# Optimization experiments

Measured on AMD Instinct MI355X. Metric: run time of the kernel, lower is better.

The kernel has to match this reference:

```python
import jax, jax.numpy as jnp
import numpy as np

B, S, D, F, E, R, K = 1, 512, 1024, 4096, 8, 16, 2
SCALING = 32.0 / 16.0  # lora_alpha / lora_r
EPS = 1e-6


def setup_inputs() -> dict:
    key = jax.random.key(0)
    ks = jax.random.split(key, 12)
    w = lambda k, shape: jax.random.normal(k, shape, dtype=jnp.float32) * 0.02
    return {
        "x": jax.random.normal(ks[0], (B, S, D), dtype=jnp.float32),
        "norm_w": jnp.ones((D,), jnp.float32),
        "w1": w(ks[1], (F, D)),      # up proj (gate branch)
        "w3": w(ks[2], (F, D)),      # up proj (value branch)
        "w2": w(ks[3], (D, F)),      # down proj
        "gate_w": w(ks[4], (E, D)),  # router
        "a1": w(ks[5], (E, R, D)), "b1": w(ks[6], (E, F, R)),
        "a3": w(ks[7], (E, R, D)), "b3": w(ks[8], (E, F, R)),
        "a2": w(ks[9], (E, R, F)), "b2": w(ks[10], (E, D, R)),
    }


def _forward(x, norm_w, w1, w3, w2, gate_w, a1, b1, a3, b3, a2, b2):
    Bq, Sq, Dq = x.shape
    # RMSNorm
    nx = x * jax.lax.rsqrt(jnp.mean(x * x, axis=-1, keepdims=True) + EPS) * norm_w
    t = nx.reshape(-1, Dq)  # [T, D] flattened tokens
    # Mixtral-style routing: softmax -> top-k -> renormalize
    probs = jax.nn.softmax(t @ gate_w.T, axis=-1)          # [T, E]
    topw, topi = jax.lax.top_k(probs, K)                   # [T, K]
    topw = topw / jnp.sum(topw, axis=-1, keepdims=True)
    weights = jnp.sum(jax.nn.one_hot(topi, E, dtype=t.dtype) * topw[..., None], axis=1)  # [T, E]
    # Shared base up-projections
    base1 = t @ w1.T  # [T, F]
    base3 = t @ w3.T  # [T, F]
    # Per-expert LoRA deltas (rank-R): [E, T, F]
    h1 = base1[None] + SCALING * jnp.einsum('etr,efr->etf', jnp.einsum('td,erd->etr', t, a1), b1)
    h3 = base3[None] + SCALING * jnp.einsum('etr,efr->etf', jnp.einsum('td,erd->etr', t, a3), b3)
    act = jax.nn.silu(h1) * h3  # SwiGLU, [E, T, F]
    # Down projection: base + per-expert LoRA -> [E, T, D]
    out_e = jnp.einsum('etf,df->etd', act, w2) \
        + SCALING * jnp.einsum('etr,edr->etd', jnp.einsum('etf,erf->etr', act, a2), b2)
    # Weighted mix over experts (weight is 0 for non-selected experts)
    out = jnp.einsum('te,etd->td', weights, out_e)
    return out.reshape(Bq, Sq, Dq)


def reference(x, norm_w, w1, w3, w2, gate_w, a1, b1, a3, b3, a2, b2):
    return _forward(x, norm_w, w1, w3, w2, gate_w, a1, b1, a3, b3, a2, b2)
```

## Files before the change

kernel.cpp:

```cpp
#include <hip/hip_runtime.h>
#include <hip/hip_bf16.h>
#include <math.h>

#define TT 512
#define DD 1024
#define FF 4096
#define EE 8
#define RR 16
#define KKSEL 2
#define SCALING 2.0f
#define EPSV 1e-6f
#define DFC 128
#define SCHUNK 32

typedef unsigned short u16;
typedef short bhalf8 __attribute__((ext_vector_type(8)));
typedef float floatx4 __attribute__((ext_vector_type(4)));
typedef unsigned short u16x8 __attribute__((ext_vector_type(8)));

__device__ __forceinline__ u16 f2b(float f) {
    unsigned x = __builtin_bit_cast(unsigned, f);
    unsigned r = (x + 0x7fffu + ((x >> 16) & 1u)) >> 16;
    return (u16)r;
}
__device__ __forceinline__ float b2f(u16 b) {
    unsigned x = ((unsigned)b) << 16;
    return __builtin_bit_cast(float, x);
}

__device__ __forceinline__ void gl_lds16(const void* g, void* l) {
    __builtin_amdgcn_global_load_lds(
        (const __attribute__((address_space(1))) void*)g,
        (__attribute__((address_space(3))) void*)l, 16, 0, 0);
}

__global__ __launch_bounds__(256) void prep_f2b_k(const float* __restrict__ x,
                                                  const float* __restrict__ nw,
                                                  const float* __restrict__ gw,
                                                  const float* __restrict__ a1,
                                                  const float* __restrict__ a3,
                                                  const float* __restrict__ w1,
                                                  const float* __restrict__ w3,
                                                  const float* __restrict__ w2,
                                                  u16* __restrict__ tb,
                                                  float* __restrict__ topw,
                                                  int* __restrict__ topi,
                                                  float* __restrict__ s1,
                                                  float* __restrict__ s3,
                                                  u16* __restrict__ wB) {
    __shared__ float tL[DD];
    __shared__ float red[12];
    __shared__ int sE[2];
    int tid = threadIdx.x;

    if (blockIdx.x >= TT) {
        const int FD = FF * DD;
        int bid = blockIdx.x - TT;
        int i = (bid * 256 + tid) * 4;
        int stride = 2048 * 256 * 4;
        for (; i < 3 * FD; i += stride) {
            int seg = i / FD, off = i - seg * FD;
            const float* src = (seg == 0) ? w1 : ((seg == 1) ? w3 : w2);
            float4 v = *(const float4*)(src + off);
            ushort4 o = { f2b(v.x), f2b(v.y), f2b(v.z), f2b(v.w) };
            *(ushort4*)(wB + i) = o;
        }
        return;
    }

    int tok = blockIdx.x;
    int wave = tid >> 6, lane = tid & 63;
    const float* xr = x + (size_t)tok * DD;
    float xv[4];
    float ss = 0.f;
    #pragma unroll
    for (int i = 0; i < 4; i++) { xv[i] = xr[tid + 256 * i]; ss += xv[i] * xv[i]; }
    #pragma unroll
    for (int o = 32; o > 0; o >>= 1) ss += __shfl_down(ss, o);
    if (lane == 0) red[wave] = ss;
    __syncthreads();
    if (tid == 0) red[8] = rsqrtf((red[0] + red[1] + red[2] + red[3]) * (1.0f / DD) + EPSV);
    __syncthreads();
    float rs = red[8];
    #pragma unroll
    for (int i = 0; i < 4; i++) {
        float v = xv[i] * rs * nw[tid + 256 * i];
        tL[tid + 256 * i] = v;
        tb[(size_t)tok * DD + tid + 256 * i] = f2b(v);
    }
    __syncthreads();
    {
        const float* g0 = gw + (size_t)(2 * wave) * DD;
        const float* g1 = g0 + DD;
        float a0 = 0.f, a1v = 0.f;
        for (int d = lane; d < DD; d += 64) {
            float tv = tL[d];
            a0 = fmaf(tv, g0[d], a0);
            a1v = fmaf(tv, g1[d], a1v);
        }
        #pragma unroll
        for (int o = 32; o > 0; o >>= 1) { a0 += __shfl_down(a0, o); a1v += __shfl_down(a1v, o); }
        if (lane == 0) { red[2 * wave] = a0; red[2 * wave + 1] = a1v; }
    }
    __syncthreads();
    if (tid == 0) {
        float m = red[0];
        #pragma unroll
        for (int e = 1; e < EE; e++) m = fmaxf(m, red[e]);
        float p[EE];
        #pragma unroll
        for (int e = 0; e < EE; e++) p[e] = expf(red[e] - m);
        int i0 = 0; float v0 = p[0];
        for (int e = 1; e < EE; e++) if (p[e] > v0) { v0 = p[e]; i0 = e; }
        int i1 = -1; float v1 = -1.f;
        for (int e = 0; e < EE; e++) { if (e == i0) continue; if (p[e] > v1) { v1 = p[e]; i1 = e; } }
        float inv = 1.f / (v0 + v1);
        topi[tok * KKSEL + 0] = i0;
        topi[tok * KKSEL + 1] = i1;
        topw[tok * KKSEL + 0] = v0 * inv;
        topw[tok * KKSEL + 1] = v1 * inv;
        sE[0] = i0; sE[1] = i1;
    }
    __syncthreads();
    {
        int half = wave >> 1, ten = wave & 1;
        int slot = tok * 2 + half;
        int e = sE[half];
        const float* ap = ten ? a3 : a1;
        float* sp = ten ? s3 : s1;
        float tv[16];
        #pragma unroll
        for (int i = 0; i < 16; i++) tv[i] = tL[lane + 64 * i];
        const float* ab = ap + (size_t)e * RR * DD;
        #pragma unroll
        for (int r = 0; r < RR; r++) {
            const float* ar = ab + (size_t)r * DD;
            float c = 0.f;
            #pragma unroll
            for (int i = 0; i < 16; i++) c = fmaf(tv[i], ar[lane + 64 * i], c);
            #pragma unroll
            for (int o = 32; o > 0; o >>= 1) c += __shfl_down(c, o);
            if (lane == 0) sp[slot * RR + r] = SCALING * c;
        }
    }
}

__global__ __launch_bounds__(256) void delta_act_k(const float* __restrict__ b1,
                                                   const float* __restrict__ b3,
                                                   const float* __restrict__ s1,
                                                   const float* __restrict__ s3,
                                                   const int* __restrict__ lists,
                                                   const int* __restrict__ counts,
                                                   const u16* __restrict__ hb,
                                                   u16* __restrict__ actb) {
    int e = blockIdx.y, f0 = blockIdx.x * DFC;
    int st = blockIdx.z * SCHUNK;
    int n = counts[e];
    if (st >= n) return;
    int gn = min(SCHUNK, n - st);
    __shared__ float bL[2][16 * 132];
    __shared__ float sG[2][SCHUNK * 16];
    __shared__ int   sSlot[SCHUNK];
    int tid = threadIdx.x;
    int g = tid >> 7, f = tid & 127;
    const int* lp = lists + e * 1024 + st;
    {
        const float* bsrc1 = b1 + ((size_t)e * FF + f0) * RR;
        const float* bsrc3 = b3 + ((size_t)e * FF + f0) * RR;
        #pragma unroll
        for (int i = tid; i < DFC * 16; i += 256) {
            int fi = i >> 4, r = i & 15;
            bL[0][r * 132 + fi] = bsrc1[i];
            bL[1][r * 132 + fi] = bsrc3[i];
        }
        int sl_l = (tid & 127) >> 2, q = tid & 3;
        if (sl_l < gn) {
            int slot = lp[sl_l];
            const float* ssrc = g ? s3 : s1;
            *(float4*)&sG[g][sl_l * 16 + q * 4] = *(const float4*)&ssrc[slot * RR + q * 4];
            if (g == 0 && q == 0) sSlot[sl_l] = slot;
        }
    }
    __syncthreads();
    for (int ii = g; ii < gn; ii += 2) {
        int slot = sSlot[ii];
        int tok = slot >> 1;
        float h1b = b2f(hb[(size_t)tok * (2 * FF) + f0 + f]);
        float h3b = b2f(hb[(size_t)tok * (2 * FF) + FF + f0 + f]);
        const float* sp1 = &sG[0][ii * 16];
        const float* sp3 = &sG[1][ii * 16];
        float d1 = 0.f, d3 = 0.f;
        #pragma unroll
        for (int r = 0; r < RR; r++) {
            d1 = fmaf(sp1[r], bL[0][r * 132 + f], d1);
            d3 = fmaf(sp3[r], bL[1][r * 132 + f], d3);
        }
        float h1 = h1b + d1, h3 = h3b + d3;
        float sig = 1.f / (1.f + expf(-h1));
        actb[(size_t)slot * FF + f0 + f] = f2b(h1 * sig * h3);
    }
}

template<int SPLITK, bool BF16OUT, bool LISTS>
__global__ __launch_bounds__(256) void gemm_nt(const u16* __restrict__ A,
                                               const u16* __restrict__ B,
                                               void* __restrict__ Cv,
                                               int M, int N, int K,
                                               const int* __restrict__ topi,
                                               int* __restrict__ lists,
                                               int* __restrict__ counts) {
    __shared__ u16 As[3][64 * 32];
    __shared__ u16 Bs[3][128 * 32];
    int tid = threadIdx.x;

    if (LISTS && blockIdx.y == gridDim.y - 1) {
        if (blockIdx.x == 0) {
            int* cnt = (int*)&As[0][0];
            if (tid < EE) cnt[tid] = 0;
            __syncthreads();
            for (int s = tid; s < TT * KKSEL; s += 256) atomicAdd(&cnt[topi[s]], 1);
            __syncthreads();
            if (tid < EE) { counts[tid] = cnt[tid]; cnt[tid] = 0; }
            __syncthreads();
            for (int s = tid; s < TT * KKSEL; s += 256) {
                int e = topi[s];
                int p = atomicAdd(&cnt[e], 1);
                lists[e * 1024 + p] = s;
            }
        }
        return;
    }

    int w = tid >> 6, lane = tid & 63;
    int wr = w >> 1, wc = w & 1;
    int lr = lane & 15, ks = lane >> 4;
    int z = (SPLITK > 1) ? blockIdx.z : 0;
    int kc = K / SPLITK;
    int k0s = z * kc;
    int nk = kc / 32;
    int m0 = blockIdx.y * 64, n0 = blockIdx.x * 128;

    int row = tid >> 2;
    int inb = (tid & 3) * 16;
    size_t rb = (size_t)K * 2;
    const char* Ag  = (const char*)A + (size_t)(m0 + row) * rb + inb + (size_t)k0s * 2;
    const char* Bg  = (const char*)B + (size_t)(n0 + row) * rb + inb + (size_t)k0s * 2;
    const char* Bg2 = Bg + 64 * rb;

    floatx4 zero4 = {0.f, 0.f, 0.f, 0.f};
    floatx4 acc[2][4];
    #pragma unroll
    for (int i = 0; i < 2; i++)
        #pragma unroll
        for (int j = 0; j < 4; j++) acc[i][j] = zero4;

    auto stage = [&](int buf, int kt) {
        size_t kb = (size_t)kt * 64;
        gl_lds16(Ag + kb, &As[buf][w * 512]);
        gl_lds16(Bg + kb, &Bs[buf][w * 512]);
        gl_lds16(Bg2 + kb, &Bs[buf][2048 + w * 512]);
    };
    auto compute = [&](int buf) {
        bhalf8 af[2], bf[4];
        #pragma unroll
        for (int i = 0; i < 2; i++)
            af[i] = *(const bhalf8*)&As[buf][(wr * 32 + i * 16 + lr) * 32 + ks * 8];
        #pragma unroll
        for (int j = 0; j < 4; j++)
            bf[j] = *(const bhalf8*)&Bs[buf][(wc * 64 + j * 16 + lr) * 32 + ks * 8];
        #pragma unroll
        for (int i = 0; i < 2; i++)
            #pragma unroll
            for (int j = 0; j < 4; j++)
                acc[i][j] = __builtin_amdgcn_mfma_f32_16x16x32_bf16(af[i], bf[j], acc[i][j], 0, 0, 0);
    };

    stage(0, 0);
    stage(1, 1);
    asm volatile("s_waitcnt vmcnt(3)" ::: "memory");
    __builtin_amdgcn_s_barrier();

    int cur = 0;
    for (int kt = 0; kt < nk; ++kt) {
        int pre = cur + 2; if (pre >= 3) pre -= 3;
        if (kt + 2 < nk) stage(pre, kt + 2);
        compute(cur);
        asm volatile("s_waitcnt lgkmcnt(0)" ::: "memory");
        if (kt + 1 < nk) {
            if (kt + 2 < nk) asm volatile("s_waitcnt vmcnt(3)" ::: "memory");
            else             asm volatile("s_waitcnt vmcnt(0)" ::: "memory");
            __builtin_amdgcn_s_barrier();
        }
        cur = (cur + 1 == 3) ? 0 : cur + 1;
    }

    int crow = (lane >> 4) * 4;
    #pragma unroll
    for (int i = 0; i < 2; i++) {
        #pragma unroll
        for (int j = 0; j < 4; j++) {
            int r0 = m0 + wr * 32 + i * 16 + crow;
            int c0 = n0 + wc * 64 + j * 16 + lr;
            if (BF16OUT) {
                u16* Cb = (u16*)Cv;
                #pragma unroll
                for (int mm = 0; mm < 4; mm++)
                    Cb[(size_t)(r0 + mm) * N + c0] = f2b(acc[i][j][mm]);
            } else {
                float* Cf = (float*)Cv + (size_t)z * M * N;
                #pragma unroll
                for (int mm = 0; mm < 4; mm++)
                    Cf[(size_t)(r0 + mm) * N + c0] = acc[i][j][mm];
            }
        }
    }
}

__global__ __launch_bounds__(256) void s2mix_k(const u16* __restrict__ actb,
                                               const float* __restrict__ a2,
                                               const int* __restrict__ topi,
                                               const float* __restrict__ topw,
                                               float* __restrict__ s2,
                                               u16* __restrict__ mixedb) {
    int tok = blockIdx.x;
    int tid = threadIdx.x, wave = tid >> 6, lane = tid & 63;
    int slot = tok * 2 + (wave >> 1);
    int e = topi[slot];
    const u16* ar = actb + (size_t)slot * FF;
    float av[64];
    #pragma unroll
    for (int i = 0; i < 16; i++) {
        ushort4 u = *(const ushort4*)(ar + lane * 4 + 256 * i);
        av[i * 4 + 0] = b2f(u.x); av[i * 4 + 1] = b2f(u.y);
        av[i * 4 + 2] = b2f(u.z); av[i * 4 + 3] = b2f(u.w);
    }
    #pragma unroll
    for (int rr = 0; rr < 8; rr++) {
        int r = (wave & 1) * 8 + rr;
        const float* a2p = a2 + ((size_t)e * RR + r) * FF;
        float c = 0.f;
        #pragma unroll
        for (int i = 0; i < 16; i++) {
            float4 w4 = *(const float4*)(a2p + lane * 4 + 256 * i);
            c = fmaf(av[i * 4 + 0], w4.x, c);
            c = fmaf(av[i * 4 + 1], w4.y, c);
            c = fmaf(av[i * 4 + 2], w4.z, c);
            c = fmaf(av[i * 4 + 3], w4.w, c);
        }
        #pragma unroll
        for (int o = 32; o > 0; o >>= 1) c += __shfl_down(c, o);
        if (lane == 0) s2[slot * RR + r] = SCALING * c;
    }
    float w0 = topw[tok * 2], w1v = topw[tok * 2 + 1];
    const u16* a0 = actb + (size_t)(tok * 2) * FF;
    const u16* a1p = a0 + FF;
    #pragma unroll
    for (int it = 0; it < 2; it++) {
        int f = tid * 8 + it * 2048;
        u16x8 v0 = *(const u16x8*)(a0 + f);
        u16x8 v1 = *(const u16x8*)(a1p + f);
        u16x8 o;
        #pragma unroll
        for (int q = 0; q < 8; q++)
            o[q] = f2b(w0 * b2f(v0[q]) + w1v * b2f(v1[q]));
        *(u16x8*)(mixedb + (size_t)tok * FF + f) = o;
    }
}

__global__ __launch_bounds__(256) void combine_k(const float* __restrict__ downP,
                                                 const float* __restrict__ s2,
                                                 const float* __restrict__ b2,
                                                 const float* __restrict__ topw,
                                                 const int* __restrict__ topi,
                                                 float* __restrict__ out) {
    int tok = blockIdx.x;
    for (int d = threadIdx.x; d < DD; d += 256) {
        float v = 0.f;
        #pragma unroll
        for (int zz = 0; zz < 8; zz++)
            v += downP[(size_t)zz * TT * DD + (size_t)tok * DD + d];
        #pragma unroll
        for (int k = 0; k < KKSEL; k++) {
            int slot = tok * KKSEL + k;
            int e = topi[slot];
            float w = topw[slot];
            const float* b2p = b2 + ((size_t)e * DD + d) * RR;
            const float* s2p = s2 + slot * RR;
            float l = 0.f;
            #pragma unroll
            for (int r = 0; r < RR; r++) l = fmaf(s2p[r], b2p[r], l);
            v += w * l;
        }
        out[(size_t)tok * DD + d] = v;
    }
}

extern "C" void kernel_launch(void* const* d_in, const int* in_sizes, int n_in,
                              void* d_out, int out_size, void* d_ws, size_t ws_size,
                              hipStream_t stream) {
    const float* x  = (const float*)d_in[0];
    const float* nw = (const float*)d_in[1];
    const float* w1 = (const float*)d_in[2];
    const float* w3 = (const float*)d_in[3];
    const float* w2 = (const float*)d_in[4];
    const float* gw = (const float*)d_in[5];
    const float* a1 = (const float*)d_in[6];
    const float* b1 = (const float*)d_in[7];
    const float* a3 = (const float*)d_in[8];
    const float* b3 = (const float*)d_in[9];
    const float* a2 = (const float*)d_in[10];
    const float* b2 = (const float*)d_in[11];
    float* out = (float*)d_out;

    float* downP = (float*)d_ws;
    float* s1    = downP + (size_t)8 * TT * DD;
    float* s3    = s1 + (size_t)TT * KKSEL * RR;
    float* s2    = s3 + (size_t)TT * KKSEL * RR;
    float* topw  = s2 + (size_t)TT * KKSEL * RR;
    int*   topi  = (int*)(topw + TT * KKSEL);
    int*   lists = topi + TT * KKSEL;
    int*   counts= lists + EE * 1024;
    u16*   tb    = (u16*)(counts + 16);
    u16*   wB    = tb + (size_t)TT * DD;
    u16*   w2b   = wB + (size_t)2 * FF * DD;
    u16*   hb    = w2b + (size_t)DD * FF;
    u16*   actb  = hb + (size_t)TT * 2 * FF;
    u16*   mixedb= actb + (size_t)TT * KKSEL * FF;

    prep_f2b_k<<<TT + 2048, 256, 0, stream>>>(
        x, nw, gw, a1, a3, w1, w3, w2, tb, topw, topi, s1, s3, wB);
    gemm_nt<1, true, true><<<dim3(2 * FF / 128, TT / 64 + 1), 256, 0, stream>>>(
        tb, wB, hb, TT, 2 * FF, DD, topi, lists, counts);
    delta_act_k<<<dim3(FF / DFC, EE, 32), 256, 0, stream>>>(
        b1, b3, s1, s3, lists, counts, hb, actb);
    s2mix_k<<<TT, 256, 0, stream>>>(actb, a2, topi, topw, s2, mixedb);
    gemm_nt<8, false, false><<<dim3(DD / 128, TT / 64, 8), 256, 0, stream>>>(
        mixedb, w2b, downP, TT, DD, FF, nullptr, nullptr, nullptr);
    combine_k<<<TT, 256, 0, stream>>>(downP, s2, b2, topw, topi, out);
}
```

Measured before the change: 99.70 us.

## Fuse fp32-to-bf16 weight conversion into GEMM B-operand loading

Removes the separate pass that converted w1, w3 and w2 to bf16 in the prep kernel. The GEMMs now read fp32 weights directly into registers, convert them to bf16 and write them into shared memory, with the K loop unrolled by two to keep the register double-buffering in step with the three-stage LDS ring. This avoids writing and re-reading about 24MB of bf16 weights. In exchange each GEMM reads twice the weight bytes and the bf16 conversion moves into the main loop, where it adds ALU work and register pressure and rewrites the wait-count pipeline.

```diff
diff --git a/kernel.cpp b/kernel.cpp
--- a/kernel.cpp
+++ b/kernel.cpp
@@ -34,42 +34,21 @@
         (__attribute__((address_space(3))) void*)l, 16, 0, 0);
 }
 
-__global__ __launch_bounds__(256) void prep_f2b_k(const float* __restrict__ x,
-                                                  const float* __restrict__ nw,
-                                                  const float* __restrict__ gw,
-                                                  const float* __restrict__ a1,
-                                                  const float* __restrict__ a3,
-                                                  const float* __restrict__ w1,
-                                                  const float* __restrict__ w3,
-                                                  const float* __restrict__ w2,
-                                                  u16* __restrict__ tb,
-                                                  float* __restrict__ topw,
-                                                  int* __restrict__ topi,
-                                                  float* __restrict__ s1,
-                                                  float* __restrict__ s3,
-                                                  u16* __restrict__ wB) {
+__global__ __launch_bounds__(256) void prep_k(const float* __restrict__ x,
+                                              const float* __restrict__ nw,
+                                              const float* __restrict__ gw,
+                                              const float* __restrict__ a1,
+                                              const float* __restrict__ a3,
+                                              u16* __restrict__ tb,
+                                              float* __restrict__ topw,
+                                              int* __restrict__ topi,
+                                              float* __restrict__ s1,
+                                              float* __restrict__ s3) {
+    int tok = blockIdx.x;
     __shared__ float tL[DD];
     __shared__ float red[12];
     __shared__ int sE[2];
-    int tid = threadIdx.x;
-
-    if (blockIdx.x >= TT) {
-        const int FD = FF * DD;
-        int bid = blockIdx.x - TT;
-        int i = (bid * 256 + tid) * 4;
-        int stride = 2048 * 256 * 4;
-        for (; i < 3 * FD; i += stride) {
-            int seg = i / FD, off = i - seg * FD;
-            const float* src = (seg == 0) ? w1 : ((seg == 1) ? w3 : w2);
-            float4 v = *(const float4*)(src + off);
-            ushort4 o = { f2b(v.x), f2b(v.y), f2b(v.z), f2b(v.w) };
-            *(ushort4*)(wB + i) = o;
-        }
-        return;
-    }
-
-    int tok = blockIdx.x;
-    int wave = tid >> 6, lane = tid & 63;
+    int tid = threadIdx.x, wave = tid >> 6, lane = tid & 63;
     const float* xr = x + (size_t)tok * DD;
     float xv[4];
     float ss = 0.f;
@@ -202,13 +181,15 @@
 }
 
 template<int SPLITK, bool BF16OUT, bool LISTS>
-__global__ __launch_bounds__(256) void gemm_nt(const u16* __restrict__ A,
-                                               const u16* __restrict__ B,
-                                               void* __restrict__ Cv,
-                                               int M, int N, int K,
-                                               const int* __restrict__ topi,
-                                               int* __restrict__ lists,
-                                               int* __restrict__ counts) {
+__global__ __launch_bounds__(256) void gemm_a16b32(const u16* __restrict__ A,
+                                                   const float* __restrict__ B0,
+                                                   const float* __restrict__ B1,
+                                                   int NS,
+                                                   void* __restrict__ Cv,
+                                                   int M, int N, int K,
+                                                   const int* __restrict__ topi,
+                                                   int* __restrict__ lists,
+                                                   int* __restrict__ counts) {
     __shared__ u16 As[3][64 * 32];
     __shared__ u16 Bs[3][128 * 32];
     int tid = threadIdx.x;
@@ -231,21 +212,18 @@
         return;
     }
 
-    int w = tid >> 6, lane = tid & 63;
-    int wr = w >> 1, wc = w & 1;
+    int wv = tid >> 6, lane = tid & 63;
+    int wr = wv >> 1, wc = wv & 1;
     int lr = lane & 15, ks = lane >> 4;
     int z = (SPLITK > 1) ? blockIdx.z : 0;
-    int kc = K / SPLITK;
-    int k0s = z * kc;
+    int kc = K / SPLITK, k0s = z * kc;
     int nk = kc / 32;
     int m0 = blockIdx.y * 64, n0 = blockIdx.x * 128;
 
-    int row = tid >> 2;
-    int inb = (tid & 3) * 16;
-    size_t rb = (size_t)K * 2;
-    const char* Ag  = (const char*)A + (size_t)(m0 + row) * rb + inb + (size_t)k0s * 2;
-    const char* Bg  = (const char*)B + (size_t)(n0 + row) * rb + inb + (size_t)k0s * 2;
-    const char* Bg2 = Bg + 64 * rb;
+    const char* Ag = (const char*)A + ((size_t)(m0 + (tid >> 2)) * K + k0s) * 2 + (tid & 3) * 16;
+    const float* Bmat = (n0 < NS) ? (B0 + (size_t)n0 * K) : (B1 + (size_t)(n0 - NS) * K);
+    const float* Bg  = Bmat + (size_t)(tid >> 2) * K + k0s + (tid & 3) * 8;
+    const float* Bg2 = Bg + (size_t)64 * K;
 
     floatx4 zero4 = {0.f, 0.f, 0.f, 0.f};
     floatx4 acc[2][4];
@@ -254,11 +232,27 @@
         #pragma unroll
         for (int j = 0; j < 4; j++) acc[i][j] = zero4;
 
-    auto stage = [&](int buf, int kt) {
-        size_t kb = (size_t)kt * 64;
-        gl_lds16(Ag + kb, &As[buf][w * 512]);
-        gl_lds16(Bg + kb, &Bs[buf][w * 512]);
-        gl_lds16(Bg2 + kb, &Bs[buf][2048 + w * 512]);
+    float4 bA[4], bB[4];
+
+    auto stageA = [&](int buf, int kt) {
+        gl_lds16(Ag + (size_t)kt * 64, &As[buf][wv * 512]);
+    };
+    auto loadB = [&](float4* r, int kt) {
+        const float* p = Bg + kt * 32;
+        const float* q = Bg2 + kt * 32;
+        r[0] = *(const float4*)(p);
+        r[1] = *(const float4*)(p + 4);
+        r[2] = *(const float4*)(q);
+        r[3] = *(const float4*)(q + 4);
+    };
+    auto writeB = [&](int buf, const float4* r) {
+        u16x8 lo, hi;
+        lo[0] = f2b(r[0].x); lo[1] = f2b(r[0].y); lo[2] = f2b(r[0].z); lo[3] = f2b(r[0].w);
+        lo[4] = f2b(r[1].x); lo[5] = f2b(r[1].y); lo[6] = f2b(r[1].z); lo[7] = f2b(r[1].w);
+        hi[0] = f2b(r[2].x); hi[1] = f2b(r[2].y); hi[2] = f2b(r[2].z); hi[3] = f2b(r[2].w);
+        hi[4] = f2b(r[3].x); hi[5] = f2b(r[3].y); hi[6] = f2b(r[3].z); hi[7] = f2b(r[3].w);
+        *(u16x8*)&Bs[buf][tid * 8] = lo;
+        *(u16x8*)&Bs[buf][2048 + tid * 8] = hi;
     };
     auto compute = [&](int buf) {
         bhalf8 af[2], bf[4];
@@ -275,23 +269,34 @@
                 acc[i][j] = __builtin_amdgcn_mfma_f32_16x16x32_bf16(af[i], bf[j], acc[i][j], 0, 0, 0);
     };
 
-    stage(0, 0);
-    stage(1, 1);
-    asm volatile("s_waitcnt vmcnt(3)" ::: "memory");
+    stageA(0, 0); loadB(bA, 0);
+    stageA(1, 1); loadB(bB, 1);
+    asm volatile("s_waitcnt vmcnt(0)" ::: "memory");
+    writeB(0, bA);
+    asm volatile("s_waitcnt lgkmcnt(0)" ::: "memory");
     __builtin_amdgcn_s_barrier();
 
     int cur = 0;
-    for (int kt = 0; kt < nk; ++kt) {
-        int pre = cur + 2; if (pre >= 3) pre -= 3;
-        if (kt + 2 < nk) stage(pre, kt + 2);
+    for (int kt = 0; kt < nk; kt += 2) {
+        int nx1 = (cur == 2) ? 0 : cur + 1;
+        int nx2 = (nx1 == 2) ? 0 : nx1 + 1;
+        if (kt + 2 < nk) { stageA(nx2, kt + 2); loadB(bA, kt + 2); }
         compute(cur);
+        if (kt + 2 < nk) asm volatile("s_waitcnt vmcnt(5)" ::: "memory");
+        else             asm volatile("s_waitcnt vmcnt(0)" ::: "memory");
+        writeB(nx1, bB);
         asm volatile("s_waitcnt lgkmcnt(0)" ::: "memory");
-        if (kt + 1 < nk) {
-            if (kt + 2 < nk) asm volatile("s_waitcnt vmcnt(3)" ::: "memory");
+        __builtin_amdgcn_s_barrier();
+        if (kt + 3 < nk) { stageA(cur, kt + 3); loadB(bB, kt + 3); }
+        compute(nx1);
+        if (kt + 2 < nk) {
+            if (kt + 3 < nk) asm volatile("s_waitcnt vmcnt(5)" ::: "memory");
             else             asm volatile("s_waitcnt vmcnt(0)" ::: "memory");
+            writeB(nx2, bA);
+            asm volatile("s_waitcnt lgkmcnt(0)" ::: "memory");
             __builtin_amdgcn_s_barrier();
         }
-        cur = (cur + 1 == 3) ? 0 : cur + 1;
+        cur = nx2;
     }
 
     int crow = (lane >> 4) * 4;
@@ -421,20 +426,17 @@
     int*   lists = topi + TT * KKSEL;
     int*   counts= lists + EE * 1024;
     u16*   tb    = (u16*)(counts + 16);
-    u16*   wB    = tb + (size_t)TT * DD;
-    u16*   w2b   = wB + (size_t)2 * FF * DD;
-    u16*   hb    = w2b + (size_t)DD * FF;
+    u16*   hb    = tb + (size_t)TT * DD;
     u16*   actb  = hb + (size_t)TT * 2 * FF;
     u16*   mixedb= actb + (size_t)TT * KKSEL * FF;
 
-    prep_f2b_k<<<TT + 2048, 256, 0, stream>>>(
-        x, nw, gw, a1, a3, w1, w3, w2, tb, topw, topi, s1, s3, wB);
-    gemm_nt<1, true, true><<<dim3(2 * FF / 128, TT / 64 + 1), 256, 0, stream>>>(
-        tb, wB, hb, TT, 2 * FF, DD, topi, lists, counts);
+    prep_k<<<TT, 256, 0, stream>>>(x, nw, gw, a1, a3, tb, topw, topi, s1, s3);
+    gemm_a16b32<1, true, true><<<dim3(2 * FF / 128, TT / 64 + 1), 256, 0, stream>>>(
+        tb, w1, w3, FF, hb, TT, 2 * FF, DD, topi, lists, counts);
     delta_act_k<<<dim3(FF / DFC, EE, 32), 256, 0, stream>>>(
         b1, b3, s1, s3, lists, counts, hb, actb);
     s2mix_k<<<TT, 256, 0, stream>>>(actb, a2, topi, topw, s2, mixedb);
-    gemm_nt<8, false, false><<<dim3(DD / 128, TT / 64, 8), 256, 0, stream>>>(
-        mixedb, w2b, downP, TT, DD, FF, nullptr, nullptr, nullptr);
+    gemm_a16b32<8, false, false><<<dim3(DD / 128, TT / 64, 8), 256, 0, stream>>>(
+        mixedb, w2, w2, DD, downP, TT, DD, FF, nullptr, nullptr, nullptr);
     combine_k<<<TT, 256, 0, stream>>>(downP, s2, b2, topw, topi, out);
 }
```

New measurement: 102.9 us. 1.03x slower.

## Move w2 bf16 conversion into first GEMM grid to overlap with compute

Applied to the files above, without the earlier changes.

The fp32-to-bf16 conversion of w2 moves out of the prep kernel into extra blocks of the first up-projection GEMM launch, so it runs alongside the matmul instead of before it. The w1/w3 conversion becomes one 8-element chunk per thread with nontemporal loads, dropping the grid-stride loop and its segment division. The intent is to shorten the serial prep kernel and hide the w2 conversion behind GEMM work. The risk is that the conversion blocks compete with the GEMM blocks for bandwidth and compute units.

```diff
diff --git a/kernel.cpp b/kernel.cpp
--- a/kernel.cpp
+++ b/kernel.cpp
@@ -12,10 +12,12 @@
 #define EPSV 1e-6f
 #define DFC 128
 #define SCHUNK 32
+#define CVTB 4096
 
 typedef unsigned short u16;
 typedef short bhalf8 __attribute__((ext_vector_type(8)));
 typedef float floatx4 __attribute__((ext_vector_type(4)));
+typedef float f32x4 __attribute__((ext_vector_type(4)));
 typedef unsigned short u16x8 __attribute__((ext_vector_type(8)));
 
 __device__ __forceinline__ u16 f2b(float f) {
@@ -41,7 +43,6 @@
                                                   const float* __restrict__ a3,
                                                   const float* __restrict__ w1,
                                                   const float* __restrict__ w3,
-                                                  const float* __restrict__ w2,
                                                   u16* __restrict__ tb,
                                                   float* __restrict__ topw,
                                                   int* __restrict__ topi,
@@ -56,15 +57,15 @@
     if (blockIdx.x >= TT) {
         const int FD = FF * DD;
         int bid = blockIdx.x - TT;
-        int i = (bid * 256 + tid) * 4;
-        int stride = 2048 * 256 * 4;
-        for (; i < 3 * FD; i += stride) {
-            int seg = i / FD, off = i - seg * FD;
-            const float* src = (seg == 0) ? w1 : ((seg == 1) ? w3 : w2);
-            float4 v = *(const float4*)(src + off);
-            ushort4 o = { f2b(v.x), f2b(v.y), f2b(v.z), f2b(v.w) };
-            *(ushort4*)(wB + i) = o;
-        }
+        int seg = bid >> 11;
+        const float* src = seg ? w3 : w1;
+        int off = (bid & 2047) * 2048 + tid * 8;
+        f32x4 v0 = __builtin_nontemporal_load((const f32x4*)(src + off));
+        f32x4 v1 = __builtin_nontemporal_load((const f32x4*)(src + off) + 1);
+        u16x8 o;
+        o[0] = f2b(v0[0]); o[1] = f2b(v0[1]); o[2] = f2b(v0[2]); o[3] = f2b(v0[3]);
+        o[4] = f2b(v1[0]); o[5] = f2b(v1[1]); o[6] = f2b(v1[2]); o[7] = f2b(v1[3]);
+        *(u16x8*)(wB + (size_t)seg * FD + off) = o;
         return;
     }
 
@@ -208,27 +209,48 @@
                                                int M, int N, int K,
                                                const int* __restrict__ topi,
                                                int* __restrict__ lists,
-                                               int* __restrict__ counts) {
+                                               int* __restrict__ counts,
+                                               const float* __restrict__ w2src,
+                                               u16* __restrict__ w2dst) {
     __shared__ u16 As[3][64 * 32];
     __shared__ u16 Bs[3][128 * 32];
     int tid = threadIdx.x;
 
-    if (LISTS && blockIdx.y == gridDim.y - 1) {
-        if (blockIdx.x == 0) {
-            int* cnt = (int*)&As[0][0];
-            if (tid < EE) cnt[tid] = 0;
-            __syncthreads();
-            for (int s = tid; s < TT * KKSEL; s += 256) atomicAdd(&cnt[topi[s]], 1);
-            __syncthreads();
-            if (tid < EE) { counts[tid] = cnt[tid]; cnt[tid] = 0; }
-            __syncthreads();
-            for (int s = tid; s < TT * KKSEL; s += 256) {
-                int e = topi[s];
-                int p = atomicAdd(&cnt[e], 1);
-                lists[e * 1024 + p] = s;
+    if (LISTS) {
+        int yrows = M / 64;
+        int by = (int)blockIdx.y;
+        if (by == yrows) {
+            if (blockIdx.x == 0) {
+                int* cnt = (int*)&As[0][0];
+                if (tid < EE) cnt[tid] = 0;
+                __syncthreads();
+                for (int s = tid; s < TT * KKSEL; s += 256) atomicAdd(&cnt[topi[s]], 1);
+                __syncthreads();
+                if (tid < EE) { counts[tid] = cnt[tid]; cnt[tid] = 0; }
+                __syncthreads();
+                for (int s = tid; s < TT * KKSEL; s += 256) {
+                    int e = topi[s];
+                    int p = atomicAdd(&cnt[e], 1);
+                    lists[e * 1024 + p] = s;
+                }
             }
-        }
-        return;
+            return;
+        }
+        if (by > yrows) {
+            int cid = (by - yrows - 1) * gridDim.x + blockIdx.x;
+            int nCvt = ((int)gridDim.y - yrows - 1) * (int)gridDim.x;
+            size_t total = (size_t)DD * FF;
+            size_t step = (size_t)nCvt * 256 * 8;
+            for (size_t i = ((size_t)cid * 256 + tid) * 8; i < total; i += step) {
+                f32x4 v0 = __builtin_nontemporal_load((const f32x4*)(w2src + i));
+                f32x4 v1 = __builtin_nontemporal_load((const f32x4*)(w2src + i) + 1);
+                u16x8 o;
+                o[0] = f2b(v0[0]); o[1] = f2b(v0[1]); o[2] = f2b(v0[2]); o[3] = f2b(v0[3]);
+                o[4] = f2b(v1[0]); o[5] = f2b(v1[1]); o[6] = f2b(v1[2]); o[7] = f2b(v1[3]);
+                *(u16x8*)(w2dst + i) = o;
+            }
+            return;
+        }
     }
 
     int w = tid >> 6, lane = tid & 63;
@@ -427,14 +449,14 @@
     u16*   actb  = hb + (size_t)TT * 2 * FF;
     u16*   mixedb= actb + (size_t)TT * KKSEL * FF;
 
-    prep_f2b_k<<<TT + 2048, 256, 0, stream>>>(
-        x, nw, gw, a1, a3, w1, w3, w2, tb, topw, topi, s1, s3, wB);
-    gemm_nt<1, true, true><<<dim3(2 * FF / 128, TT / 64 + 1), 256, 0, stream>>>(
-        tb, wB, hb, TT, 2 * FF, DD, topi, lists, counts);
+    prep_f2b_k<<<TT + CVTB, 256, 0, stream>>>(
+        x, nw, gw, a1, a3, w1, w3, tb, topw, topi, s1, s3, wB);
+    gemm_nt<1, true, true><<<dim3(2 * FF / 128, TT / 64 + 1 + 8), 256, 0, stream>>>(
+        tb, wB, hb, TT, 2 * FF, DD, topi, lists, counts, w2, w2b);
     delta_act_k<<<dim3(FF / DFC, EE, 32), 256, 0, stream>>>(
         b1, b3, s1, s3, lists, counts, hb, actb);
     s2mix_k<<<TT, 256, 0, stream>>>(actb, a2, topi, topw, s2, mixedb);
     gemm_nt<8, false, false><<<dim3(DD / 128, TT / 64, 8), 256, 0, stream>>>(
-        mixedb, w2b, downP, TT, DD, FF, nullptr, nullptr, nullptr);
+        mixedb, w2b, downP, TT, DD, FF, nullptr, nullptr, nullptr, nullptr, nullptr);
     combine_k<<<TT, 256, 0, stream>>>(downP, s2, b2, topw, topi, out);
 }
```

After: 101.8 us. 2.1% more time.
